# Kernel optimization log

Measured on AMD Instinct MI355X. Metric: run time of the kernel, lower is better.

The kernel has to match this reference:

```python
import jax, jax.numpy as jnp
import numpy as np


def setup_inputs() -> dict:
    key = jax.random.key(0)
    k1, k2, k3 = jax.random.split(key, 3)
    N = 16384
    y = jax.random.normal(k1, (N,), dtype=jnp.float32)
    y_hat = jax.random.normal(k2, (N,), dtype=jnp.float32)
    status = jax.random.randint(k3, (N,), 0, 2, dtype=jnp.int32)
    return {"y": y, "y_hat": y_hat, "status": status}


def reference(y, y_hat, status):
    # Pairwise concordance index over all pairs i < j.
    # ge[i, j] = y[i] >= y[j]; le[i, j] = y[i] <= y[j]
    N = y.shape[0]
    ge = y[:, None] >= y[None, :]
    le = y[:, None] <= y[None, :]
    ge_hat = y_hat[:, None] >= y_hat[None, :]
    le_hat = y_hat[:, None] <= y_hat[None, :]
    st_i = (status == 1)[:, None]  # astatus_1 broadcast over j
    st_j = (status == 1)[None, :]  # bstatus_1 broadcast over i
    # upper-triangular mask (strict): pairs with j > i
    mask = jnp.triu(jnp.ones((N, N), dtype=bool), k=1)

    c1 = ge & ge_hat & st_j
    c2 = le & le_hat & st_i
    cc = (c1 | c2) & mask

    tp1 = le & st_i
    tp2 = ge & st_j
    tp = (tp1 | tp2) & mask

    c = jnp.sum(cc.astype(jnp.int32)).astype(jnp.float32)
    total_pairs = jnp.sum(tp.astype(jnp.int32)).astype(jnp.float32)
    return c / total_pairs
```

## Files before the change

### kernel.cpp

```cpp
#include <hip/hip_runtime.h>


#define BLOCK 256
#define TI 256
#define TJ 512
#define GRID_MAIN 1024


__global__ __launch_bounds__(256) void compact_kernel(
    const float* __restrict__ y, const float* __restrict__ yh,
    const int* __restrict__ status, int n,
    unsigned* __restrict__ cnts,
    float* __restrict__ y1, float* __restrict__ yh1,
    float* __restrict__ y0, float* __restrict__ yh0)
{
    int i = blockIdx.x * 256 + threadIdx.x;
    int lane = threadIdx.x & 63;
    bool act = i < n;
    float yv  = act ? y[i]  : 0.0f;
    float yhv = act ? yh[i] : 0.0f;
    bool st = act && (status[i] == 1);
    unsigned long long m1 = __ballot(st);
    unsigned long long m0 = __ballot(act && !st);
    unsigned long long lt = (lane == 63) ? ~0ull >> 1 : ((1ull << lane) - 1ull);
    unsigned b1 = 0, b0 = 0;
    if (lane == 0) {
        b1 = atomicAdd(&cnts[0], (unsigned)__popcll(m1));
        b0 = atomicAdd(&cnts[1], (unsigned)__popcll(m0));
    }
    b1 = __shfl(b1, 0, 64);
    b0 = __shfl(b0, 0, 64);
    if (st) {
        unsigned s = b1 + (unsigned)__popcll(m1 & lt);
        y1[s] = yv; yh1[s] = yhv;
    } else if (act) {
        unsigned s = b0 + (unsigned)__popcll(m0 & lt);
        y0[s] = yv; yh0[s] = yhv;
    }
}

__global__ __launch_bounds__(BLOCK) void pairs_kernel(
    const unsigned* __restrict__ cnts,
    const float* __restrict__ y1, const float* __restrict__ yh1,
    const float* __restrict__ y0, const float* __restrict__ yh0,
    unsigned long long* __restrict__ acc)
{
    __shared__ __align__(16) float2 s_yy[TJ];
    const int tid = threadIdx.x;
    const unsigned K = cnts[0], M = cnts[1];
    const int ntJ  = (int)((K + TJ - 1) / TJ);
    const int ntIA = (int)((K + TI - 1) / TI);
    const int ntIB = (int)((M + TI - 1) / TI);
    const int ntA  = ntIA * ntJ;
    const int ntot = ntA + ntIB * ntJ;

    const float PINF = __int_as_float(0x7f800000);
    const float NINF = __int_as_float(0xff800000);

    unsigned accA = 0, accBc = 0, accBt = 0;

    for (int t = blockIdx.x; t < ntot; t += gridDim.x) {
        bool isA = t < ntA;
        int tt = isA ? t : t - ntA;
        int ti = tt / ntJ;
        int tj = tt - ti * ntJ;
        int jbase = tj * TJ;
        int jcnt = (int)K - jbase; if (jcnt > TJ) jcnt = TJ;

        for (int s = tid; s < TJ; s += BLOCK) {
            bool inb = s < jcnt;
            int j = jbase + s;
            float a = inb ? y1[j]  : PINF;
            float b = inb ? yh1[j] : NINF;
            s_yy[s] = make_float2(a, b);
        }
        __syncthreads();

        int i = ti * TI + tid;
        unsigned ilim = isA ? K : M;
        const float* py = isA ? y1  : y0;
        const float* ph = isA ? yh1 : yh0;
        bool iv = (unsigned)i < ilim;
        float yi  = iv ? py[i] : NINF;
        float yhi = iv ? ph[i] : NINF;

        if (isA) {
            unsigned ax = 0;
#pragma unroll 8
            for (int jj = 0; jj < TJ; ++jj) {
                float2 p = s_yy[jj];
                ax += (unsigned)((yi >= p.x) != (yhi >= p.y));
            }
            if (iv) accA += (unsigned)TJ - ax;
        } else {
            unsigned bg = 0, bc = 0;
#pragma unroll 8
            for (int jj = 0; jj < TJ; ++jj) {
                float2 p = s_yy[jj];
                bool ge = yi >= p.x;
                bool gh = yhi >= p.y;
                bg += (unsigned)ge;
                bc += (unsigned)(ge & gh);
            }
            accBt += bg; accBc += bc;
        }
        __syncthreads();
    }

#pragma unroll
    for (int off = 32; off > 0; off >>= 1) {
        accA  += __shfl_down(accA,  off, 64);
        accBc += __shfl_down(accBc, off, 64);
        accBt += __shfl_down(accBt, off, 64);
    }
    __shared__ unsigned rA[4], rC[4], rT[4];
    int wav = tid >> 6, lane = tid & 63;
    if (lane == 0) { rA[wav] = accA; rC[wav] = accBc; rT[wav] = accBt; }
    __syncthreads();
    if (tid == 0) {
        unsigned long long a = rA[0] + rA[1] + rA[2] + rA[3];
        unsigned long long c = rC[0] + rC[1] + rC[2] + rC[3];
        unsigned long long t = rT[0] + rT[1] + rT[2] + rT[3];
        if (a) atomicAdd(&acc[0], a);
        if (c) atomicAdd(&acc[1], c);
        if (t) atomicAdd(&acc[2], t);
    }
}

__global__ void finalize_kernel(const unsigned* __restrict__ cnts,
                                const unsigned long long* __restrict__ acc,
                                float* __restrict__ out)
{
    if (threadIdx.x == 0) {
        unsigned long long K = cnts[0];
        unsigned long long CC = acc[0] + 2ull * acc[1];
        unsigned long long TP = K * K + 2ull * acc[2];
        long long cn = (long long)CC - (long long)K;
        long long tn = (long long)TP - (long long)K;
        out[0] = (float)cn / (float)tn;
    }
}

extern "C" void kernel_launch(void* const* d_in, const int* in_sizes, int n_in,
                              void* d_out, int out_size, void* d_ws, size_t ws_size,
                              hipStream_t stream) {
    const float* y      = (const float*)d_in[0];
    const float* y_hat  = (const float*)d_in[1];
    const int*   status = (const int*)d_in[2];
    float* out = (float*)d_out;
    int n = in_sizes[0];

    char* base = (char*)d_ws;
    unsigned* cnts = (unsigned*)base;
    unsigned long long* acc = (unsigned long long*)(base + 8);
    float* y1  = (float*)(base + 64);
    float* yh1 = y1 + n;
    float* y0  = yh1 + n;
    float* yh0 = y0 + n;

    hipMemsetAsync(base, 0, 32, stream);

    hipLaunchKernelGGL(compact_kernel, dim3((n + 255) / 256), dim3(256), 0, stream,
                       y, y_hat, status, n, cnts, y1, yh1, y0, yh0);

    hipLaunchKernelGGL(pairs_kernel, dim3(GRID_MAIN), dim3(BLOCK), 0, stream,
                       cnts, y1, yh1, y0, yh0, acc);

    hipLaunchKernelGGL(finalize_kernel, dim3(1), dim3(64), 0, stream,
                       cnts, acc, out);
}
```

Baseline: 94.78 us.

## Unify pair counting over all i against status-1 j with deterministic compaction

Replaces the two-branch A/B formulation with one loop over all i against the compacted status-1 j set, counting ge and ge&ge_hat and deriving both totals algebraically. The atomic-based compaction becomes a deterministic prefix count over status, so the memset and the separate status-0 arrays go away. Each thread now processes two i rows per j tile (TI=512, TJ=256) to reuse each shared-memory load. Per-block partial sums go to slots reduced in a parallel finalize instead of global atomics. Risks: the prefix scan rereads status quadratically across blocks, and the total comparison work is roughly unchanged while the A path's cheaper single-compare loop is lost.

```diff
diff --git a/kernel.cpp b/kernel.cpp
--- a/kernel.cpp
+++ b/kernel.cpp
@@ -2,141 +2,140 @@
 
 
 #define BLOCK 256
-#define TI 256
-#define TJ 512
+#define TI 512
+#define TJ 256
 #define GRID_MAIN 1024
-
 
 __global__ __launch_bounds__(256) void compact_kernel(
     const float* __restrict__ y, const float* __restrict__ yh,
     const int* __restrict__ status, int n,
-    unsigned* __restrict__ cnts,
-    float* __restrict__ y1, float* __restrict__ yh1,
-    float* __restrict__ y0, float* __restrict__ yh0)
+    float2* __restrict__ jarr, unsigned* __restrict__ kout)
 {
-    int i = blockIdx.x * 256 + threadIdx.x;
-    int lane = threadIdx.x & 63;
-    bool act = i < n;
-    float yv  = act ? y[i]  : 0.0f;
-    float yhv = act ? yh[i] : 0.0f;
-    bool st = act && (status[i] == 1);
-    unsigned long long m1 = __ballot(st);
-    unsigned long long m0 = __ballot(act && !st);
-    unsigned long long lt = (lane == 63) ? ~0ull >> 1 : ((1ull << lane) - 1ull);
-    unsigned b1 = 0, b0 = 0;
-    if (lane == 0) {
-        b1 = atomicAdd(&cnts[0], (unsigned)__popcll(m1));
-        b0 = atomicAdd(&cnts[1], (unsigned)__popcll(m0));
+    const int b = blockIdx.x;
+    const int tid = threadIdx.x;
+    const int base = b * 256;
+
+    unsigned pre = 0;
+    const int4* s4 = (const int4*)status;
+    const int npre4 = base >> 2;
+    for (int k = tid; k < npre4; k += 256) {
+        int4 v = s4[k];
+        pre += (unsigned)((v.x == 1) + (v.y == 1) + (v.z == 1) + (v.w == 1));
     }
-    b1 = __shfl(b1, 0, 64);
-    b0 = __shfl(b0, 0, 64);
+#pragma unroll
+    for (int off = 32; off > 0; off >>= 1) pre += __shfl_down(pre, off, 64);
+
+    __shared__ unsigned wsum[4];
+    __shared__ unsigned wcnt[4];
+    const int wav = tid >> 6, lane = tid & 63;
+    if (lane == 0) wsum[wav] = pre;
+
+    const int i = base + tid;
+    const bool st = (i < n) && (status[i] == 1);
+    unsigned long long m = __ballot(st);
+    if (lane == 0) wcnt[wav] = (unsigned)__popcll(m);
+    __syncthreads();
+
+    const unsigned offset = wsum[0] + wsum[1] + wsum[2] + wsum[3];
+    unsigned woff = 0;
+    for (int w = 0; w < wav; ++w) woff += wcnt[w];
+    const unsigned long long lt =
+        (lane == 63) ? (~0ull >> 1) : ((1ull << lane) - 1ull);
+
     if (st) {
-        unsigned s = b1 + (unsigned)__popcll(m1 & lt);
-        y1[s] = yv; yh1[s] = yhv;
-    } else if (act) {
-        unsigned s = b0 + (unsigned)__popcll(m0 & lt);
-        y0[s] = yv; yh0[s] = yhv;
+        unsigned pos = offset + woff + (unsigned)__popcll(m & lt);
+        jarr[pos] = make_float2(y[i], yh[i]);
+    }
+    if (b == gridDim.x - 1 && tid == 0) {
+        *kout = offset + wcnt[0] + wcnt[1] + wcnt[2] + wcnt[3];
     }
 }
 
 __global__ __launch_bounds__(BLOCK) void pairs_kernel(
-    const unsigned* __restrict__ cnts,
-    const float* __restrict__ y1, const float* __restrict__ yh1,
-    const float* __restrict__ y0, const float* __restrict__ yh0,
-    unsigned long long* __restrict__ acc)
+    const unsigned* __restrict__ kout, const float2* __restrict__ jarr,
+    const float* __restrict__ y, const float* __restrict__ yh, int n,
+    unsigned* __restrict__ slots)
 {
     __shared__ __align__(16) float2 s_yy[TJ];
     const int tid = threadIdx.x;
-    const unsigned K = cnts[0], M = cnts[1];
-    const int ntJ  = (int)((K + TJ - 1) / TJ);
-    const int ntIA = (int)((K + TI - 1) / TI);
-    const int ntIB = (int)((M + TI - 1) / TI);
-    const int ntA  = ntIA * ntJ;
-    const int ntot = ntA + ntIB * ntJ;
+    unsigned K = *kout;
+    if (K > (unsigned)n) K = (unsigned)n;
+    const int ntJ = (int)((K + TJ - 1) / TJ);
+    const int ntI = (n + TI - 1) / TI;
+    const int ntot = ntI * ntJ;
 
     const float PINF = __int_as_float(0x7f800000);
     const float NINF = __int_as_float(0xff800000);
 
-    unsigned accA = 0, accBc = 0, accBt = 0;
+    unsigned bg = 0, bc = 0;
 
     for (int t = blockIdx.x; t < ntot; t += gridDim.x) {
-        bool isA = t < ntA;
-        int tt = isA ? t : t - ntA;
-        int ti = tt / ntJ;
-        int tj = tt - ti * ntJ;
-        int jbase = tj * TJ;
+        const int ti = t / ntJ;
+        const int tj = t - ti * ntJ;
+        const int jbase = tj * TJ;
         int jcnt = (int)K - jbase; if (jcnt > TJ) jcnt = TJ;
 
         for (int s = tid; s < TJ; s += BLOCK) {
-            bool inb = s < jcnt;
-            int j = jbase + s;
-            float a = inb ? y1[j]  : PINF;
-            float b = inb ? yh1[j] : NINF;
-            s_yy[s] = make_float2(a, b);
+            s_yy[s] = (s < jcnt) ? jarr[jbase + s] : make_float2(PINF, PINF);
         }
         __syncthreads();
 
-        int i = ti * TI + tid;
-        unsigned ilim = isA ? K : M;
-        const float* py = isA ? y1  : y0;
-        const float* ph = isA ? yh1 : yh0;
-        bool iv = (unsigned)i < ilim;
-        float yi  = iv ? py[i] : NINF;
-        float yhi = iv ? ph[i] : NINF;
+        const int i0 = ti * TI + tid;
+        const int i1 = i0 + BLOCK;
+        const float yi0 = (i0 < n) ? y[i0]  : NINF;
+        const float hh0 = (i0 < n) ? yh[i0] : NINF;
+        const float yi1 = (i1 < n) ? y[i1]  : NINF;
+        const float hh1 = (i1 < n) ? yh[i1] : NINF;
 
-        if (isA) {
-            unsigned ax = 0;
 #pragma unroll 8
-            for (int jj = 0; jj < TJ; ++jj) {
-                float2 p = s_yy[jj];
-                ax += (unsigned)((yi >= p.x) != (yhi >= p.y));
-            }
-            if (iv) accA += (unsigned)TJ - ax;
-        } else {
-            unsigned bg = 0, bc = 0;
-#pragma unroll 8
-            for (int jj = 0; jj < TJ; ++jj) {
-                float2 p = s_yy[jj];
-                bool ge = yi >= p.x;
-                bool gh = yhi >= p.y;
-                bg += (unsigned)ge;
-                bc += (unsigned)(ge & gh);
-            }
-            accBt += bg; accBc += bc;
+        for (int jj = 0; jj < TJ; ++jj) {
+            float2 p = s_yy[jj];
+            bool g0 = yi0 >= p.x, h0 = hh0 >= p.y;
+            bool g1 = yi1 >= p.x, h1 = hh1 >= p.y;
+            bg += (unsigned)g0 + (unsigned)g1;
+            bc += (unsigned)(g0 & h0) + (unsigned)(g1 & h1);
         }
         __syncthreads();
     }
 
 #pragma unroll
     for (int off = 32; off > 0; off >>= 1) {
-        accA  += __shfl_down(accA,  off, 64);
-        accBc += __shfl_down(accBc, off, 64);
-        accBt += __shfl_down(accBt, off, 64);
+        bg += __shfl_down(bg, off, 64);
+        bc += __shfl_down(bc, off, 64);
     }
-    __shared__ unsigned rA[4], rC[4], rT[4];
-    int wav = tid >> 6, lane = tid & 63;
-    if (lane == 0) { rA[wav] = accA; rC[wav] = accBc; rT[wav] = accBt; }
+    __shared__ unsigned rG[4], rC[4];
+    const int wav = tid >> 6, lane = tid & 63;
+    if (lane == 0) { rG[wav] = bg; rC[wav] = bc; }
     __syncthreads();
     if (tid == 0) {
-        unsigned long long a = rA[0] + rA[1] + rA[2] + rA[3];
-        unsigned long long c = rC[0] + rC[1] + rC[2] + rC[3];
-        unsigned long long t = rT[0] + rT[1] + rT[2] + rT[3];
-        if (a) atomicAdd(&acc[0], a);
-        if (c) atomicAdd(&acc[1], c);
-        if (t) atomicAdd(&acc[2], t);
+        slots[2 * blockIdx.x]     = rG[0] + rG[1] + rG[2] + rG[3];
+        slots[2 * blockIdx.x + 1] = rC[0] + rC[1] + rC[2] + rC[3];
     }
 }
 
-__global__ void finalize_kernel(const unsigned* __restrict__ cnts,
-                                const unsigned long long* __restrict__ acc,
-                                float* __restrict__ out)
+__global__ __launch_bounds__(256) void finalize_kernel(
+    const unsigned* __restrict__ kout, const unsigned* __restrict__ slots,
+    float* __restrict__ out)
 {
-    if (threadIdx.x == 0) {
-        unsigned long long K = cnts[0];
-        unsigned long long CC = acc[0] + 2ull * acc[1];
-        unsigned long long TP = K * K + 2ull * acc[2];
-        long long cn = (long long)CC - (long long)K;
-        long long tn = (long long)TP - (long long)K;
+    const int tid = threadIdx.x;
+    unsigned long long g = 0, c = 0;
+    for (int s = tid; s < GRID_MAIN; s += 256) {
+        g += slots[2 * s];
+        c += slots[2 * s + 1];
+    }
+#pragma unroll
+    for (int off = 32; off > 0; off >>= 1) {
+        g += __shfl_down(g, off, 64);
+        c += __shfl_down(c, off, 64);
+    }
+    __shared__ unsigned long long sg[4], sc[4];
+    const int wav = tid >> 6, lane = tid & 63;
+    if (lane == 0) { sg[wav] = g; sc[wav] = c; }
+    __syncthreads();
+    if (tid == 0) {
+        unsigned long long K = *kout;
+        long long cn = (long long)(sc[0] + sc[1] + sc[2] + sc[3]) - (long long)K;
+        long long tn = (long long)(sg[0] + sg[1] + sg[2] + sg[3]) - (long long)K;
         out[0] = (float)cn / (float)tn;
     }
 }
@@ -151,21 +150,16 @@
     int n = in_sizes[0];
 
     char* base = (char*)d_ws;
-    unsigned* cnts = (unsigned*)base;
-    unsigned long long* acc = (unsigned long long*)(base + 8);
-    float* y1  = (float*)(base + 64);
-    float* yh1 = y1 + n;
-    float* y0  = yh1 + n;
-    float* yh0 = y0 + n;
-
-    hipMemsetAsync(base, 0, 32, stream);
+    unsigned* kout  = (unsigned*)base;
+    unsigned* slots = (unsigned*)(base + 64);
+    float2*   jarr  = (float2*)(base + 16384);
 
     hipLaunchKernelGGL(compact_kernel, dim3((n + 255) / 256), dim3(256), 0, stream,
-                       y, y_hat, status, n, cnts, y1, yh1, y0, yh0);
+                       y, y_hat, status, n, jarr, kout);
 
     hipLaunchKernelGGL(pairs_kernel, dim3(GRID_MAIN), dim3(BLOCK), 0, stream,
-                       cnts, y1, yh1, y0, yh0, acc);
+                       kout, jarr, y, y_hat, n, slots);
 
-    hipLaunchKernelGGL(finalize_kernel, dim3(1), dim3(64), 0, stream,
-                       cnts, acc, out);
+    hipLaunchKernelGGL(finalize_kernel, dim3(1), dim3(256), 0, stream,
+                       kout, slots, out);
 }
```

Measured after the change: 82.53 us. 12.9% less time.
